# Performance work log

Hardware: AMD Instinct MI355X
Metric: run time of the kernel (lower is better)

The kernel has to match this reference:

```python
import jax, jax.numpy as jnp
import numpy as np

H, B, C, T, F = 4, 2, 64, 2048, 64   # n_head, batch, in_chan, time, n_freqs
HID = 4                               # hid_chan (per-head Q/K channels)
VD = C // H                           # per-head V channels
EPS = 1e-5


def prelu(x, a):
    return jnp.where(x >= 0, x, a * x)


def ln_cf(x, g, b):
    # LayerNormalization4D: normalize over (channel, freq) axes of (..., C, T, F)
    mu = x.mean(axis=(-3, -1), keepdims=True)
    var = ((x - mu) ** 2).mean(axis=(-3, -1), keepdims=True)
    return (x - mu) / jnp.sqrt(var + EPS) * g + b


def setup_inputs() -> dict:
    key = jax.random.key(0)
    ks = jax.random.split(key, 8)

    def w(k, shape):
        return jax.random.normal(k, shape, jnp.float32) * 0.05

    return {
        "x": jax.random.normal(ks[0], (B, C, T, F), jnp.float32),
        # per-head 1x1-conv Q/K/V projections (stacked over head axis)
        "Wq": w(ks[1], (H, HID, C)), "bq": jnp.zeros((H, HID), jnp.float32),
        "aq": jnp.full((H,), 0.25, jnp.float32),
        "gq": jnp.ones((H, HID, F), jnp.float32), "betq": jnp.zeros((H, HID, F), jnp.float32),
        "Wk": w(ks[2], (H, HID, C)), "bk": jnp.zeros((H, HID), jnp.float32),
        "ak": jnp.full((H,), 0.25, jnp.float32),
        "gk": jnp.ones((H, HID, F), jnp.float32), "betk": jnp.zeros((H, HID, F), jnp.float32),
        "Wv": w(ks[3], (H, VD, C)), "bv": jnp.zeros((H, VD), jnp.float32),
        "av": jnp.full((H,), 0.25, jnp.float32),
        "gv": jnp.ones((H, VD, F), jnp.float32), "betv": jnp.zeros((H, VD, F), jnp.float32),
        # output 1x1-conv projection
        "Wp": w(ks[4], (C, C)), "bp": jnp.zeros((C,), jnp.float32),
        "ap": jnp.full((), 0.25, jnp.float32),
        "gp": jnp.ones((C, F), jnp.float32), "betp": jnp.zeros((C, F), jnp.float32),
    }


def reference(x, Wq, bq, aq, gq, betq, Wk, bk, ak, gk, betk,
              Wv, bv, av, gv, betv, Wp, bp, ap, gp, betp):
    def qkv(W, b, a, g, be):
        # batched per-head 1x1 conv: (H,O,C) x (B,C,T,F) -> (H,B,O,T,F)
        y = jnp.einsum('hoc,bctf->hbotf', W, x) + b[:, None, :, None, None]
        y = prelu(y, a[:, None, None, None, None])
        return ln_cf(y, g[:, None, :, None, :], be[:, None, :, None, :])

    Q = qkv(Wq, bq, aq, gq, betq).reshape(H * B, HID, T, F)
    K = qkv(Wk, bk, ak, gk, betk).reshape(H * B, HID, T, F)
    V = qkv(Wv, bv, av, gv, betv).reshape(H * B, VD, T, F)

    # (HB, C', T, F) -> (HB, T, C'*F)
    Q = Q.transpose(0, 2, 1, 3).reshape(H * B, T, HID * F)
    K = K.transpose(0, 2, 1, 3).reshape(H * B, T, HID * F)
    V = V.transpose(0, 2, 1, 3).reshape(H * B, T, VD * F)

    scale = 1.0 / jnp.sqrt(jnp.asarray(HID * F, jnp.float32))
    attn = jax.nn.softmax(jnp.einsum('bqd,bkd->bqk', Q, K) * scale, axis=-1)  # (HB,T,T)
    O = jnp.einsum('bqk,bkd->bqd', attn, V)                                    # (HB,T,VD*F)

    # (HB,T,VD,F) -> (B, H*VD, T, F) matching torch head-concat order
    O = O.reshape(H * B, T, VD, F).transpose(0, 2, 1, 3)
    O = O.reshape(H, B, VD, T, F).transpose(1, 0, 2, 3, 4).reshape(B, H * VD, T, F)

    y = jnp.einsum('oc,bctf->botf', Wp, O) + bp[None, :, None, None]
    y = prelu(y, ap)
    y = ln_cf(y, gp[:, None, :], betp[:, None, :])
    return y + x
```

## Files before the change

kernel.cpp:

```cpp
#include <hip/hip_runtime.h>

#define EPS_ 1e-5f

typedef float f32x4 __attribute__((ext_vector_type(4)));
typedef short s16x8 __attribute__((ext_vector_type(8)));

static __device__ __forceinline__ short f2bf(float f) {
    unsigned u = __float_as_uint(f);
    unsigned r = (u + 0x7FFFu + ((u >> 16) & 1u)) >> 16;
    return (short)r;
}
static __device__ __forceinline__ float bf2f(short s) {
    return __uint_as_float(((unsigned)(unsigned short)s) << 16);
}

static __device__ __forceinline__ void gload16(const short* g, short* l) {
    __builtin_amdgcn_global_load_lds(
        (const __attribute__((address_space(1))) unsigned int*)g,
        (__attribute__((address_space(3))) unsigned int*)l, 16, 0, 0);
}

__global__ __launch_bounds__(256) void prep_kernel(
    const float* __restrict__ Wq, const float* __restrict__ Wk,
    const float* __restrict__ Wv, const float* __restrict__ Wp,
    short* __restrict__ Wbf, short* __restrict__ Wpbf)
{
    int i = blockIdx.x * 256 + threadIdx.x;
    if (i < 6144) {
        float v = (i < 1024) ? Wq[i] : (i < 2048 ? Wk[i - 1024] : Wv[i - 2048]);
        Wbf[i] = f2bf(v);
    } else if (i < 6144 + 4096) {
        Wpbf[i - 6144] = f2bf(Wp[i - 6144]);
    }
}

__global__ __launch_bounds__(256) void qkv_kernel(
    const float* __restrict__ x, const short* __restrict__ Wbf,
    const float* __restrict__ bq, const float* __restrict__ aq,
    const float* __restrict__ gq, const float* __restrict__ betq,
    const float* __restrict__ bk, const float* __restrict__ ak,
    const float* __restrict__ gk, const float* __restrict__ betk,
    const float* __restrict__ bv, const float* __restrict__ av,
    const float* __restrict__ gv, const float* __restrict__ betv,
    short* __restrict__ Qo, short* __restrict__ Ko, short* __restrict__ Vo)
{
    const int t = blockIdx.x;
    const int b = blockIdx.y;
    const int tid = threadIdx.x;
    const int wid = tid >> 6, lane = tid & 63;
    const int g = lane >> 4, c16 = lane & 15;
    const int f_ = tid & 63, cg = tid >> 6;

    __shared__ __align__(16) short wlds[96 * 64];
    __shared__ __align__(16) short xs[64 * 64];
    __shared__ float zs[96 * 64];
    __shared__ float stats[12][2];
    __shared__ float bias_l[96], alpha_l[96];

#pragma unroll
    for (int j = 0; j < 3; ++j) {
        int i8 = tid + 256 * j;
        int row = i8 >> 3, cb = i8 & 7;
        s16x8 v = *(const s16x8*)(Wbf + i8 * 8);
        *(s16x8*)&wlds[row * 64 + ((cb ^ (row & 7)) * 8)] = v;
    }
    if (tid < 96) {
        int row = tid; float bias, al;
        if (row < 16)      { bias = bq[row];      al = aq[row >> 2]; }
        else if (row < 32) { bias = bk[row - 16]; al = ak[(row - 16) >> 2]; }
        else               { bias = bv[row - 32]; al = av[(row - 32) >> 4]; }
        bias_l[row] = bias; alpha_l[row] = al;
    }
#pragma unroll
    for (int it = 0; it < 2; ++it) {
        int cb = cg + 4 * it, c0 = cb * 8;
        s16x8 v;
#pragma unroll
        for (int i = 0; i < 8; ++i)
            v[i] = f2bf(x[(((size_t)b * 64 + c0 + i) * 2048 + t) * 64 + f_]);
        *(s16x8*)&xs[f_ * 64 + ((cb ^ (f_ & 7)) * 8)] = v;
    }
    __syncthreads();

    const int f0 = wid * 16;
    s16x8 bfr[2];
#pragma unroll
    for (int kk = 0; kk < 2; ++kk)
        bfr[kk] = *(const s16x8*)&xs[(f0 + c16) * 64 + (((kk * 4 + g) ^ (c16 & 7)) * 8)];

    f32x4 acc[6];
#pragma unroll
    for (int rt = 0; rt < 6; ++rt) {
#pragma unroll
        for (int r = 0; r < 4; ++r) acc[rt][r] = 0.f;
#pragma unroll
        for (int kk = 0; kk < 2; ++kk) {
            s16x8 a = *(const s16x8*)&wlds[(rt * 16 + c16) * 64 + (((kk * 4 + g) ^ (c16 & 7)) * 8)];
            acc[rt] = __builtin_amdgcn_mfma_f32_16x16x32_bf16(a, bfr[kk], acc[rt], 0, 0, 0);
        }
    }

#pragma unroll
    for (int rt = 0; rt < 6; ++rt)
#pragma unroll
        for (int r = 0; r < 4; ++r) {
            int row = rt * 16 + g * 4 + r;
            float z = acc[rt][r] + bias_l[row];
            z = z >= 0.f ? z : alpha_l[row] * z;
            zs[row * 64 + f0 + c16] = z;
        }
    __syncthreads();

#pragma unroll
    for (int gi = 0; gi < 3; ++gi) {
        int grp = wid * 3 + gi;
        int base_row, n;
        if (grp < 4)      { base_row = grp * 4;             n = 256; }
        else if (grp < 8) { base_row = 16 + (grp - 4) * 4;  n = 256; }
        else              { base_row = 32 + (grp - 8) * 16; n = 1024; }
        int cnt = n >> 6;
        float s = 0.f, ss = 0.f;
        for (int i = 0; i < cnt; ++i) {
            float v = zs[(base_row + i) * 64 + lane];
            s += v; ss += v * v;
        }
#pragma unroll
        for (int msk = 32; msk >= 1; msk >>= 1) {
            s  += __shfl_xor(s, msk);
            ss += __shfl_xor(ss, msk);
        }
        if (lane == 0) {
            float mean = s / n;
            float var = ss / n - mean * mean;
            stats[grp][0] = mean;
            stats[grp][1] = rsqrtf(var + EPS_);
        }
    }
    __syncthreads();

#pragma unroll
    for (int j = 0; j < 24; ++j) {
        int row = cg + 4 * j;
        float zv = zs[row * 64 + f_];
        if (row < 16) {
            int grp = row >> 2;
            float val = (zv - stats[grp][0]) * stats[grp][1];
            val = val * gq[row * 64 + f_] + betq[row * 64 + f_];
            int h = row >> 2, o = row & 3;
            Qo[(((size_t)(h * 2 + b)) * 2048 + t) * 256 + o * 64 + f_] = f2bf(val);
        } else if (row < 32) {
            int rr = row - 16, grp = 4 + (rr >> 2);
            float val = (zv - stats[grp][0]) * stats[grp][1];
            val = val * gk[rr * 64 + f_] + betk[rr * 64 + f_];
            int h = rr >> 2, o = rr & 3;
            Ko[(((size_t)(h * 2 + b)) * 2048 + t) * 256 + o * 64 + f_] = f2bf(val);
        } else {
            int rr = row - 32, grp = 8 + (rr >> 4);
            float val = (zv - stats[grp][0]) * stats[grp][1];
            val = val * gv[rr * 64 + f_] + betv[rr * 64 + f_];
            int h = rr >> 4, ov = rr & 15;
            Vo[(((size_t)(h * 2 + b)) * 2048 + t) * 1024 + ov * 64 + f_] = f2bf(val);
        }
    }
}

__global__ __launch_bounds__(256) void vtrans_kernel(
    const short* __restrict__ Vrm, short* __restrict__ Vt)
{
    const int t0 = blockIdx.x * 64;
    const int d0 = blockIdx.y * 64;
    const int hb = blockIdx.z;
    const int tid = threadIdx.x;
    __shared__ __align__(16) short tile[64 * 72];

#pragma unroll
    for (int k = 0; k < 2; ++k) {
        int q = tid + 256 * k;
        int row = q >> 3, slot = q & 7;
        s16x8 v = *(const s16x8*)(Vrm + ((size_t)hb * 2048 + t0 + row) * 1024 + d0 + slot * 8);
        *(s16x8*)&tile[row * 72 + slot * 8] = v;
    }
    __syncthreads();
#pragma unroll
    for (int k = 0; k < 2; ++k) {
        int q = tid + 256 * k;
        int drow = q >> 3, tslot = q & 7;
        s16x8 v;
#pragma unroll
        for (int i = 0; i < 8; ++i) {
            int c = tslot * 8 + i;
            int cl = c & 31;
            int src = (c & 32) + ((cl >> 2) & 1) * 16 + ((cl >> 4) & 1) * 8
                    + ((cl >> 3) & 1) * 4 + (cl & 3);
            v[i] = tile[src * 72 + drow];
        }
        *(s16x8*)(Vt + ((size_t)hb * 1024 + d0 + drow) * 2048 + t0 + tslot * 8) = v;
    }
}

__global__ __launch_bounds__(512, 2) void attn_kernel(
    const short* __restrict__ Qg, const short* __restrict__ Kg,
    const short* __restrict__ Vt, short* __restrict__ Ob)
{
    const int hb = blockIdx.x;
    const int qt = blockIdx.y;
    const int dh = blockIdx.z;
    const int t0 = qt * 128;
    const int tid = threadIdx.x;
    const int lane = tid & 63;
    const int wq = tid >> 6;
    const int g = lane >> 4, c16 = lane & 15;

    __shared__ __align__(16) short k_lds[2][32 * 256];
    __shared__ __align__(16) short v_lds[2][512 * 32];

    const size_t kgbase = (size_t)hb * 2048 * 256;
    const size_t vgbase = ((size_t)hb * 1024 + dh * 512) * 2048;

    const size_t qrow = (size_t)hb * 2048 + t0 + wq * 16 + c16;
    s16x8 qf[8];
#pragma unroll
    for (int kf = 0; kf < 8; ++kf)
        qf[kf] = *(const s16x8*)(Qg + qrow * 256 + kf * 32 + g * 8);

    f32x4 oacc[32];
#pragma unroll
    for (int i = 0; i < 32; ++i)
#pragma unroll
        for (int r = 0; r < 4; ++r) oacc[i][r] = 0.f;

    float l_r = 0.f;

#define STAGE(buf, kt) do {                                                    \
    _Pragma("unroll")                                                          \
    for (int j_ = 0; j_ < 2; ++j_) {                                           \
        int c_ = tid + 512 * j_;                                               \
        int row_ = c_ >> 5, sp_ = c_ & 31;                                     \
        int sl_ = sp_ ^ (row_ & 7);                                            \
        gload16(Kg + kgbase + (size_t)((kt) * 32 + row_) * 256 + sl_ * 8,      \
                &k_lds[buf][c_ * 8]);                                          \
    }                                                                          \
    _Pragma("unroll")                                                          \
    for (int j_ = 0; j_ < 4; ++j_) {                                           \
        int c_ = tid + 512 * j_;                                               \
        int row_ = c_ >> 2, sp_ = c_ & 3;                                      \
        int sl_ = sp_ ^ ((row_ >> 1) & 3);                                     \
        gload16(Vt + vgbase + (size_t)row_ * 2048 + (kt) * 32 + sl_ * 8,       \
                &v_lds[buf][c_ * 8]);                                          \
    }                                                                          \
} while (0)

    STAGE(0, 0);
    __syncthreads();

    for (int t = 0; t < 64; ++t) {
        const int buf = t & 1;

        if (t < 63) STAGE(buf ^ 1, t + 1);

        f32x4 sf[2];
#pragma unroll
        for (int kt2 = 0; kt2 < 2; ++kt2)
#pragma unroll
            for (int r = 0; r < 4; ++r) sf[kt2][r] = 0.f;
        __builtin_amdgcn_s_setprio(1);
#pragma unroll
        for (int kf = 0; kf < 8; ++kf) {
#pragma unroll
            for (int kt2 = 0; kt2 < 2; ++kt2) {
                int krow = kt2 * 16 + c16;
                s16x8 ka = *(const s16x8*)&k_lds[buf]
                    [krow * 256 + (((kf * 4 + g) ^ (c16 & 7)) * 8)];
                sf[kt2] = __builtin_amdgcn_mfma_f32_16x16x32_bf16(ka, qf[kf], sf[kt2], 0, 0, 0);
            }
        }
        __builtin_amdgcn_s_setprio(0);

        float rs = 0.f;
#pragma unroll
        for (int kt2 = 0; kt2 < 2; ++kt2)
#pragma unroll
            for (int r = 0; r < 4; ++r) {
                float p = __expf(sf[kt2][r] * 0.0625f);
                sf[kt2][r] = p;
                rs += p;
            }
        rs += __shfl_xor(rs, 16);
        rs += __shfl_xor(rs, 32);
        l_r += rs;

        s16x8 pa;
#pragma unroll
        for (int e = 0; e < 8; ++e)
            pa[e] = f2bf(sf[e >> 2][e & 3]);

        __builtin_amdgcn_s_setprio(1);
#pragma unroll
        for (int dt = 0; dt < 32; ++dt) {
            s16x8 vb = *(const s16x8*)&v_lds[buf]
                [(dt * 16 + c16) * 32 + ((g ^ ((c16 >> 1) & 3)) * 8)];
            oacc[dt] = __builtin_amdgcn_mfma_f32_16x16x32_bf16(pa, vb, oacc[dt], 0, 0, 0);
        }
        __builtin_amdgcn_s_setprio(0);

        if (t < 63) __syncthreads();
    }

#undef STAGE

    float li[4];
#pragma unroll
    for (int r = 0; r < 4; ++r)
        li[r] = 1.f / __shfl(l_r, g * 4 + r);

    const int h = hb >> 1, b = hb & 1;
#pragma unroll
    for (int dt = 0; dt < 32; ++dt) {
        int vcol = dh * 512 + dt * 16 + c16;
        int cout = h * 16 + (vcol >> 6), ff = vcol & 63;
#pragma unroll
        for (int r = 0; r < 4; ++r) {
            int trow = t0 + wq * 16 + g * 4 + r;
            Ob[(((size_t)b * 64 + cout) * 2048 + trow) * 64 + ff] =
                f2bf(oacc[dt][r] * li[r]);
        }
    }
}

__global__ __launch_bounds__(256) void oproj_kernel(
    const short* __restrict__ Ob, const float* __restrict__ x,
    const short* __restrict__ Wpbf,
    const float* __restrict__ bp, const float* __restrict__ ap,
    const float* __restrict__ gp, const float* __restrict__ betp,
    float* __restrict__ out)
{
    const int t = blockIdx.x;
    const int b = blockIdx.y;
    const int tid = threadIdx.x;
    const int wid = tid >> 6, lane = tid & 63;
    const int g = lane >> 4, c16 = lane & 15;
    const int f_ = tid & 63, cg = tid >> 6;

    __shared__ __align__(16) short wp[64 * 64];
    __shared__ __align__(16) short os[64 * 64];
    __shared__ float zs[64 * 64];
    __shared__ float red[4][2];

#pragma unroll
    for (int j = 0; j < 2; ++j) {
        int i8 = tid + 256 * j;
        int row = i8 >> 3, cb = i8 & 7;
        s16x8 v = *(const s16x8*)(Wpbf + i8 * 8);
        *(s16x8*)&wp[row * 64 + ((cb ^ (row & 7)) * 8)] = v;
    }
#pragma unroll
    for (int it = 0; it < 2; ++it) {
        int cb = cg + 4 * it, c0 = cb * 8;
        s16x8 v;
#pragma unroll
        for (int i = 0; i < 8; ++i)
            v[i] = Ob[(((size_t)b * 64 + c0 + i) * 2048 + t) * 64 + f_];
        *(s16x8*)&os[f_ * 64 + ((cb ^ (f_ & 7)) * 8)] = v;
    }
    __syncthreads();

    const int f0 = wid * 16;
    s16x8 bfr[2];
#pragma unroll
    for (int kk = 0; kk < 2; ++kk)
        bfr[kk] = *(const s16x8*)&os[(f0 + c16) * 64 + (((kk * 4 + g) ^ (c16 & 7)) * 8)];

    const float ap0 = ap[0];
    f32x4 acc[4];
#pragma unroll
    for (int rt = 0; rt < 4; ++rt) {
#pragma unroll
        for (int r = 0; r < 4; ++r) acc[rt][r] = 0.f;
#pragma unroll
        for (int kk = 0; kk < 2; ++kk) {
            s16x8 a = *(const s16x8*)&wp[(rt * 16 + c16) * 64 + (((kk * 4 + g) ^ (c16 & 7)) * 8)];
            acc[rt] = __builtin_amdgcn_mfma_f32_16x16x32_bf16(a, bfr[kk], acc[rt], 0, 0, 0);
        }
    }

#pragma unroll
    for (int rt = 0; rt < 4; ++rt)
#pragma unroll
        for (int r = 0; r < 4; ++r) {
            int row = rt * 16 + g * 4 + r;
            float z = acc[rt][r] + bp[row];
            z = z >= 0.f ? z : ap0 * z;
            zs[row * 64 + f0 + c16] = z;
        }
    __syncthreads();

    float s = 0.f, ss = 0.f;
#pragma unroll
    for (int j = 0; j < 16; ++j) {
        float v = zs[(cg + 4 * j) * 64 + f_];
        s += v; ss += v * v;
    }
#pragma unroll
    for (int msk = 32; msk >= 1; msk >>= 1) {
        s  += __shfl_xor(s, msk);
        ss += __shfl_xor(ss, msk);
    }
    if (lane == 0) { red[wid][0] = s; red[wid][1] = ss; }
    __syncthreads();
    float ts  = red[0][0] + red[1][0] + red[2][0] + red[3][0];
    float tss = red[0][1] + red[1][1] + red[2][1] + red[3][1];
    float mean = ts * (1.f / 4096.f);
    float rstd = rsqrtf(tss * (1.f / 4096.f) - mean * mean + EPS_);

#pragma unroll
    for (int j = 0; j < 16; ++j) {
        int row = cg + 4 * j;
        size_t idx = (((size_t)b * 64 + row) * 2048 + t) * 64 + f_;
        out[idx] = (zs[row * 64 + f_] - mean) * rstd * gp[row * 64 + f_]
                 + betp[row * 64 + f_] + x[idx];
    }
}

extern "C" void kernel_launch(void* const* d_in, const int* in_sizes, int n_in,
                              void* d_out, int out_size, void* d_ws, size_t ws_size,
                              hipStream_t stream)
{
    const float* x    = (const float*)d_in[0];
    const float* Wq   = (const float*)d_in[1];
    const float* bq   = (const float*)d_in[2];
    const float* aq   = (const float*)d_in[3];
    const float* gq   = (const float*)d_in[4];
    const float* betq = (const float*)d_in[5];
    const float* Wk   = (const float*)d_in[6];
    const float* bk   = (const float*)d_in[7];
    const float* ak   = (const float*)d_in[8];
    const float* gk   = (const float*)d_in[9];
    const float* betk = (const float*)d_in[10];
    const float* Wv   = (const float*)d_in[11];
    const float* bv   = (const float*)d_in[12];
    const float* av   = (const float*)d_in[13];
    const float* gv   = (const float*)d_in[14];
    const float* betv = (const float*)d_in[15];
    const float* Wp   = (const float*)d_in[16];
    const float* bp   = (const float*)d_in[17];
    const float* ap   = (const float*)d_in[18];
    const float* gp   = (const float*)d_in[19];
    const float* betp = (const float*)d_in[20];

    short* Qb   = (short*)d_ws;
    short* Kb   = Qb   + (size_t)8 * 2048 * 256;
    short* Vrm  = Kb   + (size_t)8 * 2048 * 256;
    short* Vt   = Vrm  + (size_t)8 * 2048 * 1024;
    short* Obuf = Vt   + (size_t)8 * 2048 * 1024;
    short* Wbf  = Obuf + (size_t)8 * 2048 * 1024;
    short* Wpbf = Wbf  + 96 * 64;

    prep_kernel<<<40, 256, 0, stream>>>(Wq, Wk, Wv, Wp, Wbf, Wpbf);
    qkv_kernel<<<dim3(2048, 2), 256, 0, stream>>>(x, Wbf,
        bq, aq, gq, betq, bk, ak, gk, betk, bv, av, gv, betv, Qb, Kb, Vrm);
    vtrans_kernel<<<dim3(32, 16, 8), 256, 0, stream>>>(Vrm, Vt);
    attn_kernel<<<dim3(8, 16, 2), 512, 0, stream>>>(Qb, Kb, Vt, Obuf);
    oproj_kernel<<<dim3(2048, 2), 256, 0, stream>>>(Obuf, x, Wpbf,
        bp, ap, gp, betp, (float*)d_out);
}
```

Before: 247.5 us.

## Switch attention MFMAs to 32x32x16 tiles with split query/value work per wave

Replaces the 16x16x32 bf16 MFMA tiling in the attention kernel with 32x32x16 MFMAs. Each wave now handles 32 query rows and half of the 512-wide value slice, and the V transpose permutation is adjusted to match the new operand layout. The larger tiles cut the number of MFMA instructions and the LDS fragment reads per unit of work. The cost is that the QK^T scores are computed redundantly by the two wave groups sharing a query set, and the accumulator layout changes the softmax row-sum and output write indexing.

```diff
diff --git a/kernel.cpp b/kernel.cpp
--- a/kernel.cpp
+++ b/kernel.cpp
@@ -3,6 +3,7 @@
 #define EPS_ 1e-5f
 
 typedef float f32x4 __attribute__((ext_vector_type(4)));
+typedef float f32x16 __attribute__((ext_vector_type(16)));
 typedef short s16x8 __attribute__((ext_vector_type(8)));
 
 static __device__ __forceinline__ short f2bf(float f) {
@@ -190,8 +191,8 @@
         for (int i = 0; i < 8; ++i) {
             int c = tslot * 8 + i;
             int cl = c & 31;
-            int src = (c & 32) + ((cl >> 2) & 1) * 16 + ((cl >> 4) & 1) * 8
-                    + ((cl >> 3) & 1) * 4 + (cl & 3);
+            int step = (cl >> 4) & 1, hi2 = (cl >> 3) & 1, e2 = (cl >> 2) & 1, e1 = cl & 3;
+            int src = (c & 32) + 8 * (2 * step + e2) + 4 * hi2 + e1;
             v[i] = tile[src * 72 + drow];
         }
         *(s16x8*)(Vt + ((size_t)hb * 1024 + d0 + drow) * 2048 + t0 + tslot * 8) = v;
@@ -208,8 +209,10 @@
     const int t0 = qt * 128;
     const int tid = threadIdx.x;
     const int lane = tid & 63;
-    const int wq = tid >> 6;
-    const int g = lane >> 4, c16 = lane & 15;
+    const int wid = tid >> 6;
+    const int qg = wid & 3;
+    const int ds2 = wid >> 2;
+    const int q5 = lane & 31, hi = lane >> 5;
 
     __shared__ __align__(16) short k_lds[2][32 * 256];
     __shared__ __align__(16) short v_lds[2][512 * 32];
@@ -217,17 +220,17 @@
     const size_t kgbase = (size_t)hb * 2048 * 256;
     const size_t vgbase = ((size_t)hb * 1024 + dh * 512) * 2048;
 
-    const size_t qrow = (size_t)hb * 2048 + t0 + wq * 16 + c16;
-    s16x8 qf[8];
-#pragma unroll
-    for (int kf = 0; kf < 8; ++kf)
-        qf[kf] = *(const s16x8*)(Qg + qrow * 256 + kf * 32 + g * 8);
-
-    f32x4 oacc[32];
-#pragma unroll
-    for (int i = 0; i < 32; ++i)
-#pragma unroll
-        for (int r = 0; r < 4; ++r) oacc[i][r] = 0.f;
+    const size_t qrow = (size_t)hb * 2048 + t0 + qg * 32 + q5;
+    s16x8 qf[16];
+#pragma unroll
+    for (int kf = 0; kf < 16; ++kf)
+        qf[kf] = *(const s16x8*)(Qg + qrow * 256 + kf * 16 + hi * 8);
+
+    f32x16 oacc[8];
+#pragma unroll
+    for (int i = 0; i < 8; ++i)
+#pragma unroll
+        for (int r = 0; r < 16; ++r) oacc[i][r] = 0.f;
 
     float l_r = 0.f;
 
@@ -258,48 +261,49 @@
 
         if (t < 63) STAGE(buf ^ 1, t + 1);
 
-        f32x4 sf[2];
-#pragma unroll
-        for (int kt2 = 0; kt2 < 2; ++kt2)
-#pragma unroll
-            for (int r = 0; r < 4; ++r) sf[kt2][r] = 0.f;
+        f32x16 sf0, sf1;
+#pragma unroll
+        for (int r = 0; r < 16; ++r) { sf0[r] = 0.f; sf1[r] = 0.f; }
         __builtin_amdgcn_s_setprio(1);
 #pragma unroll
         for (int kf = 0; kf < 8; ++kf) {
-#pragma unroll
-            for (int kt2 = 0; kt2 < 2; ++kt2) {
-                int krow = kt2 * 16 + c16;
-                s16x8 ka = *(const s16x8*)&k_lds[buf]
-                    [krow * 256 + (((kf * 4 + g) ^ (c16 & 7)) * 8)];
-                sf[kt2] = __builtin_amdgcn_mfma_f32_16x16x32_bf16(ka, qf[kf], sf[kt2], 0, 0, 0);
-            }
+            s16x8 ka0 = *(const s16x8*)&k_lds[buf]
+                [q5 * 256 + ((((2 * kf) * 2 + hi) ^ (q5 & 7)) * 8)];
+            sf0 = __builtin_amdgcn_mfma_f32_32x32x16_bf16(ka0, qf[2 * kf], sf0, 0, 0, 0);
+            s16x8 ka1 = *(const s16x8*)&k_lds[buf]
+                [q5 * 256 + ((((2 * kf + 1) * 2 + hi) ^ (q5 & 7)) * 8)];
+            sf1 = __builtin_amdgcn_mfma_f32_32x32x16_bf16(ka1, qf[2 * kf + 1], sf1, 0, 0, 0);
         }
         __builtin_amdgcn_s_setprio(0);
 
+        float p16[16];
         float rs = 0.f;
 #pragma unroll
-        for (int kt2 = 0; kt2 < 2; ++kt2)
-#pragma unroll
-            for (int r = 0; r < 4; ++r) {
-                float p = __expf(sf[kt2][r] * 0.0625f);
-                sf[kt2][r] = p;
-                rs += p;
-            }
-        rs += __shfl_xor(rs, 16);
+        for (int r = 0; r < 16; ++r) {
+            float p = __expf((sf0[r] + sf1[r]) * 0.0625f);
+            p16[r] = p;
+            rs += p;
+        }
         rs += __shfl_xor(rs, 32);
         l_r += rs;
 
-        s16x8 pa;
-#pragma unroll
-        for (int e = 0; e < 8; ++e)
-            pa[e] = f2bf(sf[e >> 2][e & 3]);
+        s16x8 pa0, pa1;
+#pragma unroll
+        for (int e = 0; e < 8; ++e) {
+            pa0[e] = f2bf(p16[e]);
+            pa1[e] = f2bf(p16[8 + e]);
+        }
 
         __builtin_amdgcn_s_setprio(1);
 #pragma unroll
-        for (int dt = 0; dt < 32; ++dt) {
-            s16x8 vb = *(const s16x8*)&v_lds[buf]
-                [(dt * 16 + c16) * 32 + ((g ^ ((c16 >> 1) & 3)) * 8)];
-            oacc[dt] = __builtin_amdgcn_mfma_f32_16x16x32_bf16(pa, vb, oacc[dt], 0, 0, 0);
+        for (int dt = 0; dt < 8; ++dt) {
+            int rowv = ds2 * 256 + dt * 32 + q5;
+            s16x8 vb0 = *(const s16x8*)&v_lds[buf]
+                [rowv * 32 + (((0 * 2 + hi) ^ ((rowv >> 1) & 3)) * 8)];
+            oacc[dt] = __builtin_amdgcn_mfma_f32_32x32x16_bf16(pa0, vb0, oacc[dt], 0, 0, 0);
+            s16x8 vb1 = *(const s16x8*)&v_lds[buf]
+                [rowv * 32 + (((1 * 2 + hi) ^ ((rowv >> 1) & 3)) * 8)];
+            oacc[dt] = __builtin_amdgcn_mfma_f32_32x32x16_bf16(pa1, vb1, oacc[dt], 0, 0, 0);
         }
         __builtin_amdgcn_s_setprio(0);
 
@@ -308,19 +312,22 @@
 
 #undef STAGE
 
-    float li[4];
-#pragma unroll
-    for (int r = 0; r < 4; ++r)
-        li[r] = 1.f / __shfl(l_r, g * 4 + r);
+    float li[16];
+#pragma unroll
+    for (int r = 0; r < 16; ++r) {
+        int q_r = (r & 3) + 8 * (r >> 2) + 4 * hi;
+        li[r] = 1.f / __shfl(l_r, q_r);
+    }
 
     const int h = hb >> 1, b = hb & 1;
 #pragma unroll
-    for (int dt = 0; dt < 32; ++dt) {
-        int vcol = dh * 512 + dt * 16 + c16;
+    for (int dt = 0; dt < 8; ++dt) {
+        int vcol = dh * 512 + ds2 * 256 + dt * 32 + q5;
         int cout = h * 16 + (vcol >> 6), ff = vcol & 63;
 #pragma unroll
-        for (int r = 0; r < 4; ++r) {
-            int trow = t0 + wq * 16 + g * 4 + r;
+        for (int r = 0; r < 16; ++r) {
+            int q_r = (r & 3) + 8 * (r >> 2) + 4 * hi;
+            int trow = t0 + qg * 32 + q_r;
             Ob[(((size_t)b * 64 + cout) * 2048 + trow) * 64 + ff] =
                 f2bf(oacc[dt][r] * li[r]);
         }
```

Measured after the change: 291.6 us. +17.8%, slower.

## Share P tiles via LDS and split V columns across waves in attention

Applied to the files above, without the earlier changes.

Each wave now computes the softmax P tile for its own 16 query rows and writes it to a double-buffered LDS region. During PV, each wave reads all eight waves' P tiles but only a 64-column slice of V, so per-wave V LDS reads shrink by roughly eight times. K is prefetched two tiles ahead, and QK^T for the next tile is computed before PV for the current one, so the two phases overlap. The cost is extra LDS for P plus a row-sum exchange through shared memory in the epilogue, which raises LDS pressure.

```diff
diff --git a/kernel.cpp b/kernel.cpp
--- a/kernel.cpp
+++ b/kernel.cpp
@@ -208,16 +208,19 @@
     const int t0 = qt * 128;
     const int tid = threadIdx.x;
     const int lane = tid & 63;
-    const int wq = tid >> 6;
+    const int wid = tid >> 6;
     const int g = lane >> 4, c16 = lane & 15;
 
     __shared__ __align__(16) short k_lds[2][32 * 256];
     __shared__ __align__(16) short v_lds[2][512 * 32];
+    __shared__ __align__(16) short p_lds[2][8][512];
+    __shared__ float l_sh[128];
 
     const size_t kgbase = (size_t)hb * 2048 * 256;
     const size_t vgbase = ((size_t)hb * 1024 + dh * 512) * 2048;
-
-    const size_t qrow = (size_t)hb * 2048 + t0 + wq * 16 + c16;
+    const int dsl = wid * 64;
+
+    const size_t qrow = (size_t)hb * 2048 + t0 + wid * 16 + c16;
     s16x8 qf[8];
 #pragma unroll
     for (int kf = 0; kf < 8; ++kf)
@@ -231,7 +234,7 @@
 
     float l_r = 0.f;
 
-#define STAGE(buf, kt) do {                                                    \
+#define STAGE_K(buf, kt) do {                                                  \
     _Pragma("unroll")                                                          \
     for (int j_ = 0; j_ < 2; ++j_) {                                           \
         int c_ = tid + 512 * j_;                                               \
@@ -240,6 +243,9 @@
         gload16(Kg + kgbase + (size_t)((kt) * 32 + row_) * 256 + sl_ * 8,      \
                 &k_lds[buf][c_ * 8]);                                          \
     }                                                                          \
+} while (0)
+
+#define STAGE_V(buf, kt) do {                                                  \
     _Pragma("unroll")                                                          \
     for (int j_ = 0; j_ < 4; ++j_) {                                           \
         int c_ = tid + 512 * j_;                                               \
@@ -250,79 +256,97 @@
     }                                                                          \
 } while (0)
 
-    STAGE(0, 0);
+#define QKT_PHASE(nt) do {                                                     \
+    f32x4 sf0, sf1;                                                            \
+    _Pragma("unroll")                                                          \
+    for (int r = 0; r < 4; ++r) { sf0[r] = 0.f; sf1[r] = 0.f; }                \
+    __builtin_amdgcn_s_setprio(1);                                             \
+    _Pragma("unroll")                                                          \
+    for (int kf = 0; kf < 8; ++kf) {                                           \
+        int sl_ = ((kf * 4 + g) ^ (c16 & 7)) * 8;                              \
+        s16x8 ka0 = *(const s16x8*)&k_lds[(nt) & 1][c16 * 256 + sl_];          \
+        sf0 = __builtin_amdgcn_mfma_f32_16x16x32_bf16(ka0, qf[kf], sf0, 0, 0, 0); \
+        s16x8 ka1 = *(const s16x8*)&k_lds[(nt) & 1][(16 + c16) * 256 + sl_];   \
+        sf1 = __builtin_amdgcn_mfma_f32_16x16x32_bf16(ka1, qf[kf], sf1, 0, 0, 0); \
+    }                                                                          \
+    __builtin_amdgcn_s_setprio(0);                                             \
+    float rs = 0.f;                                                            \
+    _Pragma("unroll")                                                          \
+    for (int r = 0; r < 4; ++r) {                                              \
+        float p0 = __expf(sf0[r] * 0.0625f);                                   \
+        float p1 = __expf(sf1[r] * 0.0625f);                                   \
+        sf0[r] = p0; sf1[r] = p1;                                              \
+        rs += p0 + p1;                                                         \
+    }                                                                          \
+    rs += __shfl_xor(rs, 16);                                                  \
+    rs += __shfl_xor(rs, 32);                                                  \
+    l_r += rs;                                                                 \
+    s16x8 pa;                                                                  \
+    _Pragma("unroll")                                                          \
+    for (int e = 0; e < 8; ++e)                                                \
+        pa[e] = f2bf((e & 4) ? sf1[e & 3] : sf0[e & 3]);                       \
+    *(s16x8*)&p_lds[(nt) & 1][wid][lane * 8] = pa;                             \
+} while (0)
+
+    STAGE_K(0, 0);
+    __syncthreads();
+    STAGE_K(1, 1);
+    STAGE_V(0, 0);
+    QKT_PHASE(0);
     __syncthreads();
 
     for (int t = 0; t < 64; ++t) {
         const int buf = t & 1;
 
-        if (t < 63) STAGE(buf ^ 1, t + 1);
-
-        f32x4 sf[2];
-#pragma unroll
-        for (int kt2 = 0; kt2 < 2; ++kt2)
-#pragma unroll
-            for (int r = 0; r < 4; ++r) sf[kt2][r] = 0.f;
+        if (t < 62) STAGE_K(buf, t + 2);
+        if (t < 63) STAGE_V(buf ^ 1, t + 1);
+        if (t < 63) QKT_PHASE(t + 1);
+
+        s16x8 vb[4];
+#pragma unroll
+        for (int dt = 0; dt < 4; ++dt) {
+            int rowv = dsl + dt * 16 + c16;
+            vb[dt] = *(const s16x8*)&v_lds[buf][rowv * 32 + ((g ^ ((c16 >> 1) & 3)) * 8)];
+        }
         __builtin_amdgcn_s_setprio(1);
 #pragma unroll
-        for (int kf = 0; kf < 8; ++kf) {
-#pragma unroll
-            for (int kt2 = 0; kt2 < 2; ++kt2) {
-                int krow = kt2 * 16 + c16;
-                s16x8 ka = *(const s16x8*)&k_lds[buf]
-                    [krow * 256 + (((kf * 4 + g) ^ (c16 & 7)) * 8)];
-                sf[kt2] = __builtin_amdgcn_mfma_f32_16x16x32_bf16(ka, qf[kf], sf[kt2], 0, 0, 0);
+        for (int qs = 0; qs < 8; ++qs) {
+            s16x8 pa = *(const s16x8*)&p_lds[buf][qs][lane * 8];
+#pragma unroll
+            for (int dt = 0; dt < 4; ++dt)
+                oacc[qs * 4 + dt] = __builtin_amdgcn_mfma_f32_16x16x32_bf16(
+                    pa, vb[dt], oacc[qs * 4 + dt], 0, 0, 0);
+        }
+        __builtin_amdgcn_s_setprio(0);
+
+        if (t < 63) __syncthreads();
+    }
+
+#undef STAGE_K
+#undef STAGE_V
+#undef QKT_PHASE
+
+    __syncthreads();
+    if (lane < 16) l_sh[wid * 16 + lane] = l_r;
+    __syncthreads();
+
+    const int h = hb >> 1, b = hb & 1;
+#pragma unroll
+    for (int qs = 0; qs < 8; ++qs) {
+        float li[4];
+#pragma unroll
+        for (int r = 0; r < 4; ++r)
+            li[r] = 1.f / l_sh[qs * 16 + g * 4 + r];
+#pragma unroll
+        for (int dt = 0; dt < 4; ++dt) {
+            int vcol = dh * 512 + dsl + dt * 16 + c16;
+            int cout = h * 16 + (vcol >> 6), ff = vcol & 63;
+#pragma unroll
+            for (int r = 0; r < 4; ++r) {
+                int trow = t0 + qs * 16 + g * 4 + r;
+                Ob[(((size_t)b * 64 + cout) * 2048 + trow) * 64 + ff] =
+                    f2bf(oacc[qs * 4 + dt][r] * li[r]);
             }
-        }
-        __builtin_amdgcn_s_setprio(0);
-
-        float rs = 0.f;
-#pragma unroll
-        for (int kt2 = 0; kt2 < 2; ++kt2)
-#pragma unroll
-            for (int r = 0; r < 4; ++r) {
-                float p = __expf(sf[kt2][r] * 0.0625f);
-                sf[kt2][r] = p;
-                rs += p;
-            }
-        rs += __shfl_xor(rs, 16);
-        rs += __shfl_xor(rs, 32);
-        l_r += rs;
-
-        s16x8 pa;
-#pragma unroll
-        for (int e = 0; e < 8; ++e)
-            pa[e] = f2bf(sf[e >> 2][e & 3]);
-
-        __builtin_amdgcn_s_setprio(1);
-#pragma unroll
-        for (int dt = 0; dt < 32; ++dt) {
-            s16x8 vb = *(const s16x8*)&v_lds[buf]
-                [(dt * 16 + c16) * 32 + ((g ^ ((c16 >> 1) & 3)) * 8)];
-            oacc[dt] = __builtin_amdgcn_mfma_f32_16x16x32_bf16(pa, vb, oacc[dt], 0, 0, 0);
-        }
-        __builtin_amdgcn_s_setprio(0);
-
-        if (t < 63) __syncthreads();
-    }
-
-#undef STAGE
-
-    float li[4];
-#pragma unroll
-    for (int r = 0; r < 4; ++r)
-        li[r] = 1.f / __shfl(l_r, g * 4 + r);
-
-    const int h = hb >> 1, b = hb & 1;
-#pragma unroll
-    for (int dt = 0; dt < 32; ++dt) {
-        int vcol = dh * 512 + dt * 16 + c16;
-        int cout = h * 16 + (vcol >> 6), ff = vcol & 63;
-#pragma unroll
-        for (int r = 0; r < 4; ++r) {
-            int trow = t0 + wq * 16 + g * 4 + r;
-            Ob[(((size_t)b * 64 + cout) * 2048 + trow) * 64 + ff] =
-                f2bf(oacc[dt][r] * li[r]);
         }
     }
 }
```

Result: faster. 240.0 us (-3.1%).
